# Performance work log

Measured on AMD Instinct MI355X. Metric: run time of the kernel, lower is better.

## Reference

```python
import jax, jax.numpy as jnp
import numpy as np

DIN = 2048
DOUT = 2048
NUM_HEADS = 16
HEAD_DIM = DIN // NUM_HEADS  # 128
BLOCK_SIZE = 2048
ROPE_THETA = 10000.0


def precompute_freqs(block_size, head_dim):
    inv_freq = 1.0 / (ROPE_THETA ** (jnp.arange(0, head_dim, 2, dtype=jnp.float32) / head_dim))
    t = jnp.arange(block_size, dtype=jnp.float32)
    freqs = jnp.outer(t, inv_freq)  # [S, head_dim//2]
    return jnp.cos(freqs), jnp.sin(freqs)


def apply_rotary_emb(x, cos, sin):
    # x: [B, S, H, D]; cos/sin: [S, D//2]
    xr = x.reshape(*x.shape[:-1], -1, 2)  # pairs of consecutive dims (complex view)
    x1, x2 = xr[..., 0], xr[..., 1]
    c = cos[None, :, None, :]
    s = sin[None, :, None, :]
    o1 = x1 * c - x2 * s
    o2 = x1 * s + x2 * c
    return jnp.stack([o1, o2], axis=-1).reshape(x.shape)


def setup_inputs() -> dict:
    key = jax.random.key(0)
    k1, k2, k3 = jax.random.split(key, 3)
    x = jax.random.normal(k1, (2, 2048, DIN), dtype=jnp.float32)
    Wqkv = jax.random.normal(k2, (DIN, 3 * DOUT), dtype=jnp.float32) * (DIN ** -0.5)
    Wproj = jax.random.normal(k3, (DIN, DOUT), dtype=jnp.float32) * (DIN ** -0.5)
    return {"x": x, "Wqkv": Wqkv, "Wproj": Wproj}


def reference(x, Wqkv, Wproj):
    B, S, _ = x.shape
    cos, sin = precompute_freqs(BLOCK_SIZE, HEAD_DIM)
    cos, sin = cos[:S], sin[:S]
    qkv = x @ Wqkv  # [B, S, 3*DOUT]
    q, k, v = jnp.split(qkv, 3, axis=-1)
    q = q.reshape(B, S, NUM_HEADS, HEAD_DIM)
    k = k.reshape(B, S, NUM_HEADS, HEAD_DIM)
    v = v.reshape(B, S, NUM_HEADS, HEAD_DIM)
    q = apply_rotary_emb(q, cos, sin)
    k = apply_rotary_emb(k, cos, sin)
    # causal SDPA with scale 1/sqrt(head_dim)
    scale = HEAD_DIM ** -0.5
    scores = jnp.einsum('bqhd,bkhd->bhqk', q, k) * scale
    causal = jnp.tril(jnp.ones((S, S), dtype=bool))
    scores = jnp.where(causal[None, None], scores, jnp.finfo(scores.dtype).min)
    attn = jax.nn.softmax(scores, axis=-1)
    y = jnp.einsum('bhqk,bkhd->bqhd', attn, v).reshape(B, S, DOUT)
    return y @ Wproj
```

## Files before the change

kernel.cpp:

```cpp
#include <hip/hip_runtime.h>

#define DIN 2048
#define NH 16
#define DH 128
#define SEQ 2048
#define BB 2
#define N3 6144
#define MM 4096

typedef __bf16 bf16;
typedef __attribute__((ext_vector_type(8))) __bf16 bf16x8;
typedef __attribute__((ext_vector_type(4))) __bf16 bf16x4;
typedef __attribute__((ext_vector_type(4))) float f32x4;

__device__ __forceinline__ f32x4 mfma16(bf16x8 a, bf16x8 b, f32x4 c) {
  return __builtin_amdgcn_mfma_f32_16x16x32_bf16(a, b, c, 0, 0, 0);
}

__device__ __forceinline__ void async16(const void* g, void* l) {
  __builtin_amdgcn_global_load_lds((const __attribute__((address_space(1))) void*)g,
                                   (__attribute__((address_space(3))) void*)l, 16, 0, 0);
}

__global__ void sniff_k(const unsigned short* __restrict__ x, int* __restrict__ flag) {
  __shared__ int cnt;
  if (threadIdx.x == 0) cnt = 0;
  __syncthreads();
  unsigned short u = x[threadIdx.x * 2];
  int e = (u >> 7) & 0xff;
  if (e >= 108 && e <= 140) atomicAdd(&cnt, 1);
  __syncthreads();
  if (threadIdx.x == 0) *flag = (cnt >= 128) ? 1 : 0;
}

__global__ __launch_bounds__(256) void cast_x_k(const void* __restrict__ in, bf16* __restrict__ out,
                                                const int* __restrict__ flag) {
  size_t i = ((size_t)blockIdx.x * 256 + threadIdx.x) * 8;
  if (*flag) {
    *(bf16x8*)(out + i) = *(const bf16x8*)((const bf16*)in + i);
  } else {
    const float* f = (const float*)in;
    bf16x8 v;
    for (int j = 0; j < 8; j++) v[j] = (bf16)f[i + j];
    *(bf16x8*)(out + i) = v;
  }
}

__global__ __launch_bounds__(256) void cast_wT_k(const void* __restrict__ in, bf16* __restrict__ out,
                                                 const int* __restrict__ flag, int R, int C) {
  __shared__ float t[32][33];
  int c0 = blockIdx.x * 32, r0 = blockIdx.y * 32;
  int tx = threadIdx.x & 31, ty = threadIdx.x >> 5;
  bool isb = *flag != 0;
  for (int j = 0; j < 4; j++) {
    int r = ty + j * 8;
    size_t idx = (size_t)(r0 + r) * C + c0 + tx;
    float v = isb ? (float)((const bf16*)in)[idx] : ((const float*)in)[idx];
    t[r][tx] = v;
  }
  __syncthreads();
  for (int j = 0; j < 4; j++) {
    int c = ty + j * 8;
    out[(size_t)(c0 + c) * R + r0 + tx] = (bf16)t[tx][c];
  }
}

__global__ __launch_bounds__(256) void gemm_qkv_k(const bf16* __restrict__ A, const bf16* __restrict__ BT,
                                                  bf16* __restrict__ Qb, bf16* __restrict__ Kb,
                                                  bf16* __restrict__ Vb) {
  __shared__ __align__(16) bf16 As[128 * 64];
  __shared__ __align__(16) bf16 Bs[128 * 64];
  const int K = DIN;
  int m0 = blockIdx.y * 128, n0 = blockIdx.x * 128;
  int tid = threadIdx.x, w = tid >> 6, l = tid & 63;
  int l15 = l & 15, quad = l >> 4;
  int wm = (w & 1) * 64, wn = (w >> 1) * 64;
  f32x4 zero = {0.f, 0.f, 0.f, 0.f};
  f32x4 acc[4][4];
  for (int i = 0; i < 4; i++)
    for (int j = 0; j < 4; j++) acc[i][j] = zero;
  int gch = (l & 7) ^ (l >> 3);
  const bf16* Ag = A + (size_t)(m0 + w * 32 + (l >> 3)) * K + gch * 8;
  const bf16* Bg = BT + (size_t)(n0 + w * 32 + (l >> 3)) * K + gch * 8;
  bf16* AsW = As + w * 2048;
  bf16* BsW = Bs + w * 2048;
  for (int k0 = 0; k0 < K; k0 += 64) {
    __syncthreads();
    for (int j = 0; j < 4; j++) async16(Ag + k0 + (size_t)j * 8 * K, AsW + j * 512);
    for (int j = 0; j < 4; j++) async16(Bg + k0 + (size_t)j * 8 * K, BsW + j * 512);
    __syncthreads();
    for (int kk = 0; kk < 2; kk++) {
      bf16x8 af[4], bfv[4];
      for (int i = 0; i < 4; i++)
        af[i] = *(const bf16x8*)&As[(wm + i * 16 + l15) * 64 + (((kk * 4 + quad) ^ (l15 & 7)) << 3)];
      for (int j = 0; j < 4; j++)
        bfv[j] = *(const bf16x8*)&Bs[(wn + j * 16 + l15) * 64 + (((kk * 4 + quad) ^ (l15 & 7)) << 3)];
      for (int i = 0; i < 4; i++)
        for (int j = 0; j < 4; j++) acc[i][j] = mfma16(af[i], bfv[j], acc[i][j]);
    }
  }
  for (int j = 0; j < 4; j++) {
    int col = n0 + wn + j * 16 + l15;
    int part = col >> 11, cw = col & 2047;
    int h = cw >> 7, d = cw & 127;
    bf16* dst = (part == 0) ? Qb : ((part == 1) ? Kb : Vb);
    for (int i = 0; i < 4; i++) {
      int mrow = m0 + wm + i * 16 + quad * 4;
      for (int r = 0; r < 4; r++) {
        int m = mrow + r;
        int b = m >> 11, s = m & 2047;
        int dd = (part == 1) ? (((((d >> 3) ^ (s & 7)) << 3)) | (d & 7)) : d;
        dst[(((size_t)(b * NH + h)) * SEQ + s) * DH + dd] = (bf16)acc[i][j][r];
      }
    }
  }
}

__global__ __launch_bounds__(256) void rope_k(bf16* __restrict__ Qb, bf16* __restrict__ Kb) {
  int i = blockIdx.x * 256 + threadIdx.x;
  int d2 = i & 63;
  int s = (i >> 6) & 2047;
  int bh = i >> 17;
  int dl = 2 * d2;
  float invf = expf(-9.210340371976184f * (float)dl * (1.0f / 128.0f));
  float ang = (float)s * invf;
  float sn, cs;
  sincosf(ang, &sn, &cs);
  size_t row = ((size_t)bh * SEQ + s) * DH;
  const float scale = 0.08838834764831845f * 1.4426950408889634f;
  size_t qb = row + dl;
  float q1 = (float)Qb[qb], q2 = (float)Qb[qb + 1];
  Qb[qb] = (bf16)((q1 * cs - q2 * sn) * scale);
  Qb[qb + 1] = (bf16)((q1 * sn + q2 * cs) * scale);
  size_t kb = row + ((((dl >> 3) ^ (s & 7)) << 3) | (dl & 7));
  float k1 = (float)Kb[kb], k2 = (float)Kb[kb + 1];
  Kb[kb] = (bf16)(k1 * cs - k2 * sn);
  Kb[kb + 1] = (bf16)(k1 * sn + k2 * cs);
}

__global__ __launch_bounds__(256) void transpose_v_k(const bf16* __restrict__ V, bf16* __restrict__ Vt) {
  __shared__ float t[32][33];
  int s0 = blockIdx.x * 32, d0 = blockIdx.y * 32;
  int bh = blockIdx.z;
  const bf16* Vp = V + (size_t)bh * SEQ * DH;
  bf16* Vo = Vt + (size_t)bh * DH * SEQ;
  int tx = threadIdx.x & 31, ty = threadIdx.x >> 5;
  for (int j = 0; j < 4; j++)
    t[ty + j * 8][tx] = (float)Vp[(size_t)(s0 + ty + j * 8) * DH + d0 + tx];
  __syncthreads();
  for (int j = 0; j < 4; j++) {
    int dh = d0 + ty + j * 8;
    int s = s0 + tx;
    int sl = s & 63;
    int col = (s & ~63) | ((((sl >> 3) ^ (dh & 7)) << 3) | (sl & 7));
    Vo[(size_t)dh * SEQ + col] = (bf16)t[tx][ty + j * 8];
  }
}

__global__ __launch_bounds__(256, 2) void attn_k(const bf16* __restrict__ Qb, const bf16* __restrict__ Kb,
                                                 const bf16* __restrict__ Vt, bf16* __restrict__ Yb) {
  __shared__ __align__(16) bf16 Ks[2][64 * 128];
  __shared__ __align__(16) bf16 Vs[2][128 * 64];
  __shared__ __align__(16) bf16 Pl[4][16 * 76];
  int bh = blockIdx.x;
  int slot = blockIdx.y;
  int w = threadIdx.x >> 6, l = threadIdx.x & 63;
  int l15 = l & 15, quad = l >> 4;
  const bf16* Qp = Qb + (size_t)bh * SEQ * DH;
  const bf16* Kp = Kb + (size_t)bh * SEQ * DH;
  const bf16* Vp = Vt + (size_t)bh * DH * SEQ;
  int b = bh >> 4, h = bh & 15;
  f32x4 zero = {0.f, 0.f, 0.f, 0.f};
  bf16* P = &Pl[w][0];

  auto stage = [&](int it, int buf) {
    const char* gk = (const char*)Kp + (size_t)it * 16384 + w * 4096 + l * 16;
    char* lk = (char*)&Ks[buf][0] + w * 4096;
    for (int i = 0; i < 4; i++) async16(gk + i * 1024, lk + i * 1024);
    const char* gv = (const char*)Vp + (size_t)it * 128 + (size_t)(w * 32 + (l >> 3)) * (SEQ * 2) + (l & 7) * 16;
    char* lv = (char*)&Vs[buf][0] + w * 32 * 128;
    for (int i = 0; i < 4; i++) async16(gv + (size_t)i * 8 * (SEQ * 2), lv + i * 1024);
  };

  int tiles[2] = {31 - slot, slot};
  for (int half = 0; half < 2; half++) {
    int tile = tiles[half];
    int qw = tile * 64 + w * 16;
    bf16x8 qf[4];
    for (int kc = 0; kc < 4; kc++)
      qf[kc] = *(const bf16x8*)&Qp[(size_t)(qw + l15) * DH + kc * 32 + quad * 8];
    f32x4 o[8];
    for (int ns = 0; ns < 8; ns++) o[ns] = zero;
    float mprev = -1e30f, lsum = 0.f;
    int nkt = tile + 1;

    stage(0, 0);
    __syncthreads();
    for (int it = 0; it < nkt; it++) {
      int buf = it & 1;
      bool more = (it + 1 < nkt);
      asm volatile("s_waitcnt vmcnt(4)" ::: "memory");
      __builtin_amdgcn_s_barrier();
      __builtin_amdgcn_sched_barrier(0);
      if (more) stage(it + 1, buf ^ 1);
      int k0 = it * 64;
      f32x4 st[4];
      for (int ns = 0; ns < 4; ns++) st[ns] = zero;
      for (int kc = 0; kc < 4; kc++)
        for (int ns = 0; ns < 4; ns++) {
          bf16x8 kf = *(const bf16x8*)&Ks[buf][(ns * 16 + l15) * 128 + (((kc * 4 + quad) ^ (l15 & 7)) << 3)];
          st[ns] = mfma16(kf, qf[kc], st[ns]);
        }
      int qq = qw + l15;
      if (k0 + 63 > qw) {
        for (int ns = 0; ns < 4; ns++) {
          int kk = k0 + ns * 16 + quad * 4;
          for (int r = 0; r < 4; r++)
            if (kk + r > qq) st[ns][r] = -1e30f;
        }
      }
      float pm = -1e30f;
      for (int ns = 0; ns < 4; ns++)
        for (int r = 0; r < 4; r++) pm = fmaxf(pm, st[ns][r]);
      pm = fmaxf(pm, __shfl_xor(pm, 16, 64));
      pm = fmaxf(pm, __shfl_xor(pm, 32, 64));
      float mnew = fmaxf(mprev, pm);
      float al = exp2f(mprev - mnew);
      mprev = mnew;
      float ps = 0.f;
      for (int ns = 0; ns < 4; ns++)
        for (int r = 0; r < 4; r++) {
          float e = exp2f(st[ns][r] - mnew);
          st[ns][r] = e;
          ps += e;
        }
      ps += __shfl_xor(ps, 16, 64);
      ps += __shfl_xor(ps, 32, 64);
      lsum = lsum * al + ps;
      for (int ns = 0; ns < 8; ns++) o[ns] *= al;
      for (int ns = 0; ns < 4; ns++) {
        bf16x4 pk;
        for (int r = 0; r < 4; r++) pk[r] = (bf16)st[ns][r];
        *(bf16x4*)&P[l15 * 76 + ns * 16 + quad * 4] = pk;
      }
      asm volatile("s_waitcnt lgkmcnt(0)" ::: "memory");
      bf16x8 pa[2];
      for (int kc = 0; kc < 2; kc++)
        pa[kc] = *(const bf16x8*)&P[l15 * 76 + kc * 32 + quad * 8];
      if (more) {
        asm volatile("s_waitcnt vmcnt(8)" ::: "memory");
      } else {
        asm volatile("s_waitcnt vmcnt(0)" ::: "memory");
      }
      __builtin_amdgcn_s_barrier();
      __builtin_amdgcn_sched_barrier(0);
      for (int ns = 0; ns < 8; ns++)
        for (int kc = 0; kc < 2; kc++) {
          bf16x8 vf = *(const bf16x8*)&Vs[buf][(ns * 16 + l15) * 64 + (((kc * 4 + quad) ^ (l15 & 7)) << 3)];
          o[ns] = mfma16(vf, pa[kc], o[ns]);
        }
    }
    __syncthreads();
    float inv = 1.0f / lsum;
    int q = qw + l15;
    size_t base = ((size_t)(b * SEQ + q)) * DIN + h * DH + quad * 4;
    for (int ns = 0; ns < 8; ns++) {
      bf16x4 pk;
      for (int r = 0; r < 4; r++) pk[r] = (bf16)(o[ns][r] * inv);
      *(bf16x4*)&Yb[base + ns * 16] = pk;
    }
  }
}

__global__ __launch_bounds__(256) void gemm_proj_k(const bf16* __restrict__ A, const bf16* __restrict__ BT,
                                                   void* __restrict__ out, const int* __restrict__ flag) {
  __shared__ __align__(16) bf16 As[128 * 64];
  __shared__ __align__(16) bf16 Bs[128 * 64];
  const int K = DIN;
  int m0 = blockIdx.y * 128, n0 = blockIdx.x * 128;
  int tid = threadIdx.x, w = tid >> 6, l = tid & 63;
  int l15 = l & 15, quad = l >> 4;
  int wm = (w & 1) * 64, wn = (w >> 1) * 64;
  bool obf = *flag != 0;
  f32x4 zero = {0.f, 0.f, 0.f, 0.f};
  f32x4 acc[4][4];
  for (int i = 0; i < 4; i++)
    for (int j = 0; j < 4; j++) acc[i][j] = zero;
  int gch = (l & 7) ^ (l >> 3);
  const bf16* Ag = A + (size_t)(m0 + w * 32 + (l >> 3)) * K + gch * 8;
  const bf16* Bg = BT + (size_t)(n0 + w * 32 + (l >> 3)) * K + gch * 8;
  bf16* AsW = As + w * 2048;
  bf16* BsW = Bs + w * 2048;
  for (int k0 = 0; k0 < K; k0 += 64) {
    __syncthreads();
    for (int j = 0; j < 4; j++) async16(Ag + k0 + (size_t)j * 8 * K, AsW + j * 512);
    for (int j = 0; j < 4; j++) async16(Bg + k0 + (size_t)j * 8 * K, BsW + j * 512);
    __syncthreads();
    for (int kk = 0; kk < 2; kk++) {
      bf16x8 af[4], bfv[4];
      for (int i = 0; i < 4; i++)
        af[i] = *(const bf16x8*)&As[(wm + i * 16 + l15) * 64 + (((kk * 4 + quad) ^ (l15 & 7)) << 3)];
      for (int j = 0; j < 4; j++)
        bfv[j] = *(const bf16x8*)&Bs[(wn + j * 16 + l15) * 64 + (((kk * 4 + quad) ^ (l15 & 7)) << 3)];
      for (int i = 0; i < 4; i++)
        for (int j = 0; j < 4; j++) acc[i][j] = mfma16(af[i], bfv[j], acc[i][j]);
    }
  }
  for (int j = 0; j < 4; j++) {
    int col = n0 + wn + j * 16 + l15;
    for (int i = 0; i < 4; i++) {
      int mrow = m0 + wm + i * 16 + quad * 4;
      for (int r = 0; r < 4; r++) {
        size_t idx = (size_t)(mrow + r) * DIN + col;
        float v = acc[i][j][r];
        if (obf)
          ((bf16*)out)[idx] = (bf16)v;
        else
          ((float*)out)[idx] = v;
      }
    }
  }
}

extern "C" void kernel_launch(void* const* d_in, const int* in_sizes, int n_in,
                              void* d_out, int out_size, void* d_ws, size_t ws_size,
                              hipStream_t stream) {
  char* ws = (char*)d_ws;
  int* flag = (int*)ws;
  bf16* Xb = (bf16*)(ws + 256);
  bf16* WqkvT = (bf16*)(ws + 256 + 16777216);
  bf16* WprojT = (bf16*)(ws + 256 + 16777216 + 25165824);
  bf16* Qb = (bf16*)(ws + 256 + 16777216 + 25165824 + 8388608);
  bf16* Kb = Qb + (size_t)MM * DIN;
  bf16* Vb = Kb + (size_t)MM * DIN;
  bf16* Vt = Vb + (size_t)MM * DIN;
  bf16* Yb = Xb;

  sniff_k<<<1, 256, 0, stream>>>((const unsigned short*)d_in[0], flag);
  cast_x_k<<<4096, 256, 0, stream>>>(d_in[0], Xb, flag);
  cast_wT_k<<<dim3(192, 64), 256, 0, stream>>>(d_in[1], WqkvT, flag, DIN, N3);
  cast_wT_k<<<dim3(64, 64), 256, 0, stream>>>(d_in[2], WprojT, flag, DIN, DIN);
  gemm_qkv_k<<<dim3(48, 32), 256, 0, stream>>>(Xb, WqkvT, Qb, Kb, Vb);
  rope_k<<<16384, 256, 0, stream>>>(Qb, Kb);
  transpose_v_k<<<dim3(64, 4, 32), 256, 0, stream>>>(Vb, Vt);
  attn_k<<<dim3(32, 16), 256, 0, stream>>>(Qb, Kb, Vt, Yb);
  gemm_proj_k<<<dim3(16, 32), 256, 0, stream>>>(Yb, WprojT, d_out, flag);
}
```

Measured before the change: 397.3 us.

## Fuse V transpose into QKV GEMM epilogue, vectorize weight-transpose stores, raise MFMA priority

The QKV GEMM epilogue now writes V straight into the transposed, swizzled Vt layout using packed 4-wide bf16 stores, so the separate transpose_v_k kernel and its extra pass through V in global memory are gone. The weight cast/transpose kernel now writes pairs of bf16 per thread instead of single elements, which cuts the number of narrow global stores. The attention kernel wraps its two MFMA loops in s_setprio so those waves are favored when issuing matrix instructions. The V stores are strided by SEQ across lanes and may coalesce poorly.

```diff
diff --git a/kernel.cpp b/kernel.cpp
--- a/kernel.cpp
+++ b/kernel.cpp
@@ -11,6 +11,7 @@
 typedef __bf16 bf16;
 typedef __attribute__((ext_vector_type(8))) __bf16 bf16x8;
 typedef __attribute__((ext_vector_type(4))) __bf16 bf16x4;
+typedef __attribute__((ext_vector_type(2))) __bf16 bf16x2;
 typedef __attribute__((ext_vector_type(4))) float f32x4;
 
 __device__ __forceinline__ f32x4 mfma16(bf16x8 a, bf16x8 b, f32x4 c) {
@@ -59,15 +60,20 @@
     t[r][tx] = v;
   }
   __syncthreads();
-  for (int j = 0; j < 4; j++) {
-    int c = ty + j * 8;
-    out[(size_t)(c0 + c) * R + r0 + tx] = (bf16)t[tx][c];
+  int tx8 = threadIdx.x & 15;
+  int cy = threadIdx.x >> 4;
+  for (int j = 0; j < 2; j++) {
+    int c = cy + j * 16;
+    bf16x2 v;
+    v[0] = (bf16)t[2 * tx8][c];
+    v[1] = (bf16)t[2 * tx8 + 1][c];
+    *(bf16x2*)&out[(size_t)(c0 + c) * R + r0 + 2 * tx8] = v;
   }
 }
 
 __global__ __launch_bounds__(256) void gemm_qkv_k(const bf16* __restrict__ A, const bf16* __restrict__ BT,
                                                   bf16* __restrict__ Qb, bf16* __restrict__ Kb,
-                                                  bf16* __restrict__ Vb) {
+                                                  bf16* __restrict__ Vt) {
   __shared__ __align__(16) bf16 As[128 * 64];
   __shared__ __align__(16) bf16 Bs[128 * 64];
   const int K = DIN;
@@ -103,14 +109,25 @@
     int col = n0 + wn + j * 16 + l15;
     int part = col >> 11, cw = col & 2047;
     int h = cw >> 7, d = cw & 127;
-    bf16* dst = (part == 0) ? Qb : ((part == 1) ? Kb : Vb);
-    for (int i = 0; i < 4; i++) {
-      int mrow = m0 + wm + i * 16 + quad * 4;
-      for (int r = 0; r < 4; r++) {
-        int m = mrow + r;
-        int b = m >> 11, s = m & 2047;
-        int dd = (part == 1) ? (((((d >> 3) ^ (s & 7)) << 3)) | (d & 7)) : d;
-        dst[(((size_t)(b * NH + h)) * SEQ + s) * DH + dd] = (bf16)acc[i][j][r];
+    if (part < 2) {
+      bf16* dst = (part == 0) ? Qb : Kb;
+      for (int i = 0; i < 4; i++) {
+        int mrow = m0 + wm + i * 16 + quad * 4;
+        for (int r = 0; r < 4; r++) {
+          int m = mrow + r;
+          int b = m >> 11, s = m & 2047;
+          int dd = (part == 1) ? ((((d >> 3) ^ (s & 7)) << 3) | (d & 7)) : d;
+          dst[(((size_t)(b * NH + h)) * SEQ + s) * DH + dd] = (bf16)acc[i][j][r];
+        }
+      }
+    } else {
+      for (int i = 0; i < 4; i++) {
+        int mrow = m0 + wm + i * 16 + quad * 4;
+        int b = mrow >> 11, s = mrow & 2047;
+        int scol = (s & ~63) | (((((s >> 3) & 7) ^ (d & 7)) << 3) | (s & 7));
+        bf16x4 pk;
+        for (int r = 0; r < 4; r++) pk[r] = (bf16)acc[i][j][r];
+        *(bf16x4*)&Vt[((size_t)(b * NH + h) * DH + d) * SEQ + scol] = pk;
       }
     }
   }
@@ -138,25 +155,6 @@
   Kb[kb + 1] = (bf16)(k1 * sn + k2 * cs);
 }
 
-__global__ __launch_bounds__(256) void transpose_v_k(const bf16* __restrict__ V, bf16* __restrict__ Vt) {
-  __shared__ float t[32][33];
-  int s0 = blockIdx.x * 32, d0 = blockIdx.y * 32;
-  int bh = blockIdx.z;
-  const bf16* Vp = V + (size_t)bh * SEQ * DH;
-  bf16* Vo = Vt + (size_t)bh * DH * SEQ;
-  int tx = threadIdx.x & 31, ty = threadIdx.x >> 5;
-  for (int j = 0; j < 4; j++)
-    t[ty + j * 8][tx] = (float)Vp[(size_t)(s0 + ty + j * 8) * DH + d0 + tx];
-  __syncthreads();
-  for (int j = 0; j < 4; j++) {
-    int dh = d0 + ty + j * 8;
-    int s = s0 + tx;
-    int sl = s & 63;
-    int col = (s & ~63) | ((((sl >> 3) ^ (dh & 7)) << 3) | (sl & 7));
-    Vo[(size_t)dh * SEQ + col] = (bf16)t[tx][ty + j * 8];
-  }
-}
-
 __global__ __launch_bounds__(256, 2) void attn_k(const bf16* __restrict__ Qb, const bf16* __restrict__ Kb,
                                                  const bf16* __restrict__ Vt, bf16* __restrict__ Yb) {
   __shared__ __align__(16) bf16 Ks[2][64 * 128];
@@ -206,11 +204,13 @@
       int k0 = it * 64;
       f32x4 st[4];
       for (int ns = 0; ns < 4; ns++) st[ns] = zero;
+      __builtin_amdgcn_s_setprio(1);
       for (int kc = 0; kc < 4; kc++)
         for (int ns = 0; ns < 4; ns++) {
           bf16x8 kf = *(const bf16x8*)&Ks[buf][(ns * 16 + l15) * 128 + (((kc * 4 + quad) ^ (l15 & 7)) << 3)];
           st[ns] = mfma16(kf, qf[kc], st[ns]);
         }
+      __builtin_amdgcn_s_setprio(0);
       int qq = qw + l15;
       if (k0 + 63 > qw) {
         for (int ns = 0; ns < 4; ns++) {
@@ -254,11 +254,13 @@
       }
       __builtin_amdgcn_s_barrier();
       __builtin_amdgcn_sched_barrier(0);
+      __builtin_amdgcn_s_setprio(1);
       for (int ns = 0; ns < 8; ns++)
         for (int kc = 0; kc < 2; kc++) {
           bf16x8 vf = *(const bf16x8*)&Vs[buf][(ns * 16 + l15) * 64 + (((kc * 4 + quad) ^ (l15 & 7)) << 3)];
           o[ns] = mfma16(vf, pa[kc], o[ns]);
         }
+      __builtin_amdgcn_s_setprio(0);
     }
     __syncthreads();
     float inv = 1.0f / lsum;
@@ -340,9 +342,8 @@
   cast_x_k<<<4096, 256, 0, stream>>>(d_in[0], Xb, flag);
   cast_wT_k<<<dim3(192, 64), 256, 0, stream>>>(d_in[1], WqkvT, flag, DIN, N3);
   cast_wT_k<<<dim3(64, 64), 256, 0, stream>>>(d_in[2], WprojT, flag, DIN, DIN);
-  gemm_qkv_k<<<dim3(48, 32), 256, 0, stream>>>(Xb, WqkvT, Qb, Kb, Vb);
+  gemm_qkv_k<<<dim3(48, 32), 256, 0, stream>>>(Xb, WqkvT, Qb, Kb, Vt);
   rope_k<<<16384, 256, 0, stream>>>(Qb, Kb);
-  transpose_v_k<<<dim3(64, 4, 32), 256, 0, stream>>>(Vb, Vt);
   attn_k<<<dim3(32, 16), 256, 0, stream>>>(Qb, Kb, Vt, Yb);
   gemm_proj_k<<<dim3(16, 32), 256, 0, stream>>>(Yb, WprojT, d_out, flag);
 }
```

Measured after the change: 395.7 us. No clear change (-0.4%).
